# Performance work log

Measured on AMD Instinct MI355X. Metric: run time of the kernel, lower is better.

Reference implementation:

```python
import jax, jax.numpy as jnp
import numpy as np

N_USERS = 100000
N_ITEMS = 50000
D = 64
N_LAYERS = 3
E_RAW = 2_000_000
B = 4096


def setup_inputs() -> dict:
    rng = np.random.RandomState(0)
    u = rng.randint(0, N_USERS, E_RAW).astype(np.int64)
    i = rng.randint(0, N_ITEMS, E_RAW).astype(np.int64)
    lin = np.unique(u * N_ITEMS + i)  # dedupe interactions like the dok_matrix would
    u = (lin // N_ITEMS).astype(np.int32)
    i = (lin % N_ITEMS).astype(np.int32)
    deg_u = np.bincount(u, minlength=N_USERS).astype(np.float64)
    deg_i = np.bincount(i, minlength=N_ITEMS).astype(np.float64)
    inv_u = np.where(deg_u > 0, 1.0 / np.sqrt(np.maximum(deg_u, 1.0)), 0.0)
    inv_i = np.where(deg_i > 0, 1.0 / np.sqrt(np.maximum(deg_i, 1.0)), 0.0)
    val = (inv_u[u] * inv_i[i]).astype(np.float32)  # D^-1/2 A D^-1/2 entries
    # symmetric bipartite Laplacian: user block rows then item block rows
    rows = np.concatenate([u, i + N_USERS]).astype(np.int32)
    cols = np.concatenate([i + N_USERS, u]).astype(np.int32)
    vals = np.concatenate([val, val])

    key = jax.random.key(0)
    k1, k2, k3, k4 = jax.random.split(key, 4)
    embeds = jax.random.normal(k1, (N_USERS + N_ITEMS, D), jnp.float32) * 0.1
    users = jax.random.randint(k2, (B,), 0, N_USERS)
    pos_items = jax.random.randint(k3, (B,), 0, N_ITEMS)
    neg_items = jax.random.randint(k4, (B,), 0, N_ITEMS)
    return dict(embeds=embeds, vals=jnp.asarray(vals), rows=jnp.asarray(rows),
                cols=jnp.asarray(cols), users=users, pos_items=pos_items,
                neg_items=neg_items)


def reference(embeds, vals, rows, cols, users, pos_items, neg_items):
    N = N_USERS + N_ITEMS
    cur = embeds
    acc = embeds  # running sum over layer embeddings (incl. layer 0)
    for _ in range(N_LAYERS):
        msg = vals[:, None] * cur[cols]                      # [nnz, D] gather
        cur = jax.ops.segment_sum(msg, rows, num_segments=N)  # SpMM scatter-add
        acc = acc + cur
    mean = acc / (N_LAYERS + 1)
    user_e = mean[:N_USERS]
    item_e = mean[N_USERS:]
    return user_e[users], item_e[pos_items], item_e[neg_items]
```

## Files before the change

### kernel.cpp

```cpp
#include <hip/hip_runtime.h>
#include <hip/hip_bf16.h>

#define N_USERS 100000
#define N_ITEMS 50000
#define N_TOT   150000
#define D       64
#define NBUCK   ((N_ITEMS + 127) >> 7)
#define BCAP    6144
#define CONVU_B 391
#define FLAG_B  48

typedef float v2f __attribute__((ext_vector_type(2)));

__device__ __forceinline__ unsigned bf16rn(float f) {
    unsigned x = __float_as_uint(f);
    return (x + 0x7FFFu + ((x >> 16) & 1u)) >> 16;
}
__device__ __forceinline__ unsigned packbf(float a, float b) {
    return bf16rn(a) | (bf16rn(b) << 16);
}
__device__ __forceinline__ int lower_bound(const int* __restrict__ a, int n, int key) {
    int lo = 0, hi = n;
    while (lo < hi) {
        int mid = (lo + hi) >> 1;
        if (a[mid] < key) lo = mid + 1; else hi = mid;
    }
    return lo;
}

__global__ __launch_bounds__(256) void preA_kernel(
        const float* __restrict__ embeds, const int* __restrict__ rows,
        const int* __restrict__ cols, int* __restrict__ user_ptr,
        unsigned* __restrict__ ebfS, float* __restrict__ invrow,
        const int* __restrict__ users, const int* __restrict__ pos,
        const int* __restrict__ neg, unsigned char* __restrict__ flags,
        int* __restrict__ ccur, int* __restrict__ tmp,
        unsigned short* __restrict__ cols16, int E, int B) {
    int b = blockIdx.x, t = threadIdx.x;
    if (b < CONVU_B) {
        __shared__ int ptr_s[257];
        __shared__ float inv_s[256];
        int base = b * 256;
        int r = base + t;
        int v = lower_bound(rows, E, r);
        ptr_s[t] = v;
        if (r <= N_USERS) user_ptr[r] = v;
        if (t == 0) ptr_s[256] = lower_bound(rows, E, base + 256);
        __syncthreads();
        if (r < N_USERS) {
            int deg = ptr_s[t + 1] - ptr_s[t];
            float inv = (deg > 0) ? (float)(1.0 / sqrt((double)deg)) : 0.f;
            inv_s[t] = inv;
            invrow[r] = inv;
        } else inv_s[t] = 0.f;
        __syncthreads();
        int fl = t & 15;
        #pragma unroll
        for (int i = 0; i < 16; ++i) {
            int lr = i * 16 + (t >> 4);
            int row = base + lr;
            if (row < N_USERS) {
                float inv = inv_s[lr];
                float4 v4 = *(const float4*)(embeds + (size_t)row * D + fl * 4);
                uint2 o;
                o.x = packbf(inv * v4.x, inv * v4.y);
                o.y = packbf(inv * v4.z, inv * v4.w);
                *(uint2*)(ebfS + (size_t)row * 32 + fl * 2) = o;
            }
        }
    } else if (b < CONVU_B + FLAG_B) {
        int k = (b - CONVU_B) * 256 + t;
        if (k < 3 * B) {
            int row;
            if (k < B)          row = users[k];
            else if (k < 2 * B) row = N_USERS + pos[k - B];
            else                row = N_USERS + neg[k - 2 * B];
            flags[row] = 1;
        }
    } else {
        __shared__ int cnt[NBUCK];
        __shared__ int basep[NBUCK];
        const int K = 16;
        int chunk = (b - CONVU_B - FLAG_B) * (256 * K);
        for (int i = t; i < NBUCK; i += 256) cnt[i] = 0;
        __syncthreads();
        int pk[K]; int bk[K];
        #pragma unroll
        for (int k = 0; k < K; ++k) {
            int e = chunk + k * 256 + t;
            if (e < E) {
                int i = cols[e] - N_USERS;
                cols16[e] = (unsigned short)i;
                bk[k] = i >> 7;
                pk[k] = ((i & 127) << 17) | rows[e];
                atomicAdd(&cnt[bk[k]], 1);
            } else bk[k] = -1;
        }
        __syncthreads();
        for (int i = t; i < NBUCK; i += 256) {
            int c = cnt[i];
            basep[i] = c ? atomicAdd(&ccur[i], c) : 0;
            cnt[i] = 0;
        }
        __syncthreads();
        #pragma unroll
        for (int k = 0; k < K; ++k) {
            if (bk[k] >= 0) {
                int pos2 = basep[bk[k]] + atomicAdd(&cnt[bk[k]], 1);
                if (pos2 < BCAP)
                    tmp[(size_t)bk[k] * BCAP + pos2] = pk[k];
            }
        }
    }
}

__global__ __launch_bounds__(256) void preB_kernel(
        const int* __restrict__ tmp, const int* __restrict__ ccur,
        const float* __restrict__ embeds,
        int* __restrict__ item_beg, int* __restrict__ item_end,
        int* __restrict__ nbr, unsigned* __restrict__ ebfS,
        unsigned* __restrict__ bb1, float* __restrict__ invrow) {
    int b = blockIdx.x, t = threadIdx.x;
    if (b == NBUCK) {
        if (t < 16) {
            *(uint2*)(ebfS + (size_t)N_TOT * 32 + t * 2) = make_uint2(0u, 0u);
            *(uint2*)(bb1  + (size_t)N_TOT * 32 + t * 2) = make_uint2(0u, 0u);
        }
        if (t == 0) invrow[N_TOT] = 0.f;
        return;
    }
    __shared__ int stage[BCAP];
    __shared__ int hist[128];
    __shared__ int scn[128];
    __shared__ int curs[128];
    __shared__ float inv_s[128];
    int n = ccur[b]; if (n > BCAP) n = BCAP;
    const int* src = tmp + (size_t)b * BCAP;
    if (t < 128) hist[t] = 0;
    __syncthreads();
    for (int p = t; p < n; p += 256) {
        int q = src[p];
        stage[p] = q;
        atomicAdd(&hist[q >> 17], 1);
    }
    __syncthreads();
    if (t < 128) scn[t] = hist[t];
    __syncthreads();
    for (int off = 1; off < 128; off <<= 1) {
        int x = (t < 128 && t >= off) ? scn[t - off] : 0;
        __syncthreads();
        if (t < 128) scn[t] += x;
        __syncthreads();
    }
    if (t < 128) {
        int excl = scn[t] - hist[t];
        curs[t] = excl;
        int gi = (b << 7) + t;
        float inv = (hist[t] > 0) ? (float)(1.0 / sqrt((double)hist[t])) : 0.f;
        inv_s[t] = inv;
        if (gi < N_ITEMS) {
            item_beg[gi] = b * BCAP + excl;
            item_end[gi] = b * BCAP + excl + hist[t];
            invrow[N_USERS + gi] = inv;
        }
    }
    __syncthreads();
    int* dst = nbr + (size_t)b * BCAP;
    for (int p = t; p < n; p += 256) {
        int q = stage[p];
        int pos = atomicAdd(&curs[q >> 17], 1);
        dst[pos] = q & 0x1FFFF;
    }
    int fl = t & 15;
    #pragma unroll
    for (int i = 0; i < 8; ++i) {
        int lr = i * 16 + (t >> 4);
        int gi = (b << 7) + lr;
        if (gi < N_ITEMS) {
            int row = N_USERS + gi;
            float inv = inv_s[lr];
            float4 v4 = *(const float4*)(embeds + (size_t)row * D + fl * 4);
            uint2 o;
            o.x = packbf(inv * v4.x, inv * v4.y);
            o.y = packbf(inv * v4.z, inv * v4.w);
            *(uint2*)(ebfS + (size_t)row * 32 + fl * 2) = o;
        }
    }
}

__global__ __launch_bounds__(256) void agg_kernel(
        const unsigned* __restrict__ gsrc,
        float* __restrict__ nxt, unsigned* __restrict__ nxtb,
        const float* __restrict__ invrow,
        const unsigned char* __restrict__ flags,
        const int* __restrict__ user_ptr, const unsigned short* __restrict__ cols16,
        const int* __restrict__ item_beg, const int* __restrict__ item_end,
        const int* __restrict__ nbr) {
    int wave = (int)((blockIdx.x * blockDim.x + threadIdx.x) >> 6);
    int lane = (int)(threadIdx.x & 63);
    if (wave >= N_TOT) return;
    int g  = lane >> 3;
    int fl = lane & 7;

    bool is_user = wave < N_USERS;
    int s, epos, dummy;
    const unsigned* sb;
    if (is_user) {
        s = user_ptr[wave]; epos = user_ptr[wave + 1];
        sb = gsrc + (size_t)N_USERS * 32; dummy = N_ITEMS;
    } else {
        int i = wave - N_USERS; s = item_beg[i]; epos = item_end[i];
        sb = gsrc; dummy = N_TOT;
    }

    v2f a0 = {0.f, 0.f}, a1 = {0.f, 0.f}, a2 = {0.f, 0.f}, a3 = {0.f, 0.f};

    for (int base = s; base < epos; base += 64) {
        int cnt = epos - base; if (cnt > 64) cnt = 64;
        int col = dummy;
        if (lane < cnt)
            col = is_user ? (int)cols16[base + lane] : nbr[base + lane];
        int tcount = (cnt + 7) >> 3;
        #pragma unroll 4
        for (int t = 0; t < tcount; ++t) {
            int c = __shfl(col, 8 * t + g);
            uint4 q = *(const uint4*)(sb + (size_t)c * 32 + fl * 4);
            v2f p0 = {__uint_as_float(q.x << 16), __uint_as_float(q.x & 0xFFFF0000u)};
            v2f p1 = {__uint_as_float(q.y << 16), __uint_as_float(q.y & 0xFFFF0000u)};
            v2f p2 = {__uint_as_float(q.z << 16), __uint_as_float(q.z & 0xFFFF0000u)};
            v2f p3 = {__uint_as_float(q.w << 16), __uint_as_float(q.w & 0xFFFF0000u)};
            a0 += p0; a1 += p1; a2 += p2; a3 += p3;
        }
    }
    float acc[8] = {a0.x, a0.y, a1.x, a1.y, a2.x, a2.y, a3.x, a3.y};
    #pragma unroll
    for (int j = 0; j < 8; ++j) {
        acc[j] += __shfl_xor(acc[j], 8);
        acc[j] += __shfl_xor(acc[j], 16);
        acc[j] += __shfl_xor(acc[j], 32);
    }
    if (lane < 8) {
        float inv = invrow[wave];
        float f[8];
        #pragma unroll
        for (int j = 0; j < 8; ++j) f[j] = inv * acc[j];
        uint4 o;
        o.x = packbf(inv * f[0], inv * f[1]); o.y = packbf(inv * f[2], inv * f[3]);
        o.z = packbf(inv * f[4], inv * f[5]); o.w = packbf(inv * f[6], inv * f[7]);
        *(uint4*)(nxtb + (size_t)wave * 32 + fl * 4) = o;
        if (flags[wave]) {
            size_t ro = (size_t)wave * D + fl * 8;
            *(float4*)(nxt + ro)     = make_float4(f[0], f[1], f[2], f[3]);
            *(float4*)(nxt + ro + 4) = make_float4(f[4], f[5], f[6], f[7]);
        }
    }
}

__global__ __launch_bounds__(256) void agg3_fused_kernel(
        const unsigned* __restrict__ gsrc,
        const float* __restrict__ e0, const float* __restrict__ e1,
        const float* __restrict__ e2, const float* __restrict__ invrow,
        const int* __restrict__ users, const int* __restrict__ pos,
        const int* __restrict__ neg,
        const int* __restrict__ user_ptr, const unsigned short* __restrict__ cols16,
        const int* __restrict__ item_beg, const int* __restrict__ item_end,
        const int* __restrict__ nbr,
        float* __restrict__ out, int B) {
    int slot = (int)((blockIdx.x * blockDim.x + threadIdx.x) >> 6);
    int lane = (int)(threadIdx.x & 63);
    if (slot >= 3 * B) return;
    int g  = lane >> 3;
    int fl = lane & 7;

    int row;
    if (slot < B)          row = users[slot];
    else if (slot < 2 * B) row = N_USERS + pos[slot - B];
    else                   row = N_USERS + neg[slot - 2 * B];

    bool is_user = row < N_USERS;
    int s, epos, dummy;
    const unsigned* sb;
    if (is_user) {
        s = user_ptr[row]; epos = user_ptr[row + 1];
        sb = gsrc + (size_t)N_USERS * 32; dummy = N_ITEMS;
    } else {
        int i = row - N_USERS; s = item_beg[i]; epos = item_end[i];
        sb = gsrc; dummy = N_TOT;
    }

    v2f a0 = {0.f, 0.f}, a1 = {0.f, 0.f}, a2 = {0.f, 0.f}, a3 = {0.f, 0.f};

    for (int base = s; base < epos; base += 64) {
        int cnt = epos - base; if (cnt > 64) cnt = 64;
        int col = dummy;
        if (lane < cnt)
            col = is_user ? (int)cols16[base + lane] : nbr[base + lane];
        int tcount = (cnt + 7) >> 3;
        #pragma unroll 4
        for (int t = 0; t < tcount; ++t) {
            int c = __shfl(col, 8 * t + g);
            uint4 q = *(const uint4*)(sb + (size_t)c * 32 + fl * 4);
            v2f p0 = {__uint_as_float(q.x << 16), __uint_as_float(q.x & 0xFFFF0000u)};
            v2f p1 = {__uint_as_float(q.y << 16), __uint_as_float(q.y & 0xFFFF0000u)};
            v2f p2 = {__uint_as_float(q.z << 16), __uint_as_float(q.z & 0xFFFF0000u)};
            v2f p3 = {__uint_as_float(q.w << 16), __uint_as_float(q.w & 0xFFFF0000u)};
            a0 += p0; a1 += p1; a2 += p2; a3 += p3;
        }
    }
    float acc[8] = {a0.x, a0.y, a1.x, a1.y, a2.x, a2.y, a3.x, a3.y};
    #pragma unroll
    for (int j = 0; j < 8; ++j) {
        acc[j] += __shfl_xor(acc[j], 8);
        acc[j] += __shfl_xor(acc[j], 16);
        acc[j] += __shfl_xor(acc[j], 32);
    }
    if (lane < 8) {
        float inv = invrow[row];
        size_t ro = (size_t)row * D + fl * 8;
        float4 x0 = *(const float4*)(e0 + ro), x1 = *(const float4*)(e0 + ro + 4);
        float4 y0 = *(const float4*)(e1 + ro), y1 = *(const float4*)(e1 + ro + 4);
        float4 z0 = *(const float4*)(e2 + ro), z1 = *(const float4*)(e2 + ro + 4);
        float4 r0, r1;
        r0.x = (x0.x + y0.x + z0.x + inv * acc[0]) * 0.25f;
        r0.y = (x0.y + y0.y + z0.y + inv * acc[1]) * 0.25f;
        r0.z = (x0.z + y0.z + z0.z + inv * acc[2]) * 0.25f;
        r0.w = (x0.w + y0.w + z0.w + inv * acc[3]) * 0.25f;
        r1.x = (x1.x + y1.x + z1.x + inv * acc[4]) * 0.25f;
        r1.y = (x1.y + y1.y + z1.y + inv * acc[5]) * 0.25f;
        r1.z = (x1.z + y1.z + z1.z + inv * acc[6]) * 0.25f;
        r1.w = (x1.w + y1.w + z1.w + inv * acc[7]) * 0.25f;
        size_t oo = (size_t)slot * D + fl * 8;
        *(float4*)(out + oo)     = r0;
        *(float4*)(out + oo + 4) = r1;
    }
}

extern "C" void kernel_launch(void* const* d_in, const int* in_sizes, int n_in,
                              void* d_out, int out_size, void* d_ws, size_t ws_size,
                              hipStream_t stream) {
    const float* embeds = (const float*)d_in[0];
    const int*   rows   = (const int*)d_in[2];
    const int*   cols   = (const int*)d_in[3];
    const int*   users  = (const int*)d_in[4];
    const int*   pos    = (const int*)d_in[5];
    const int*   neg    = (const int*)d_in[6];
    const int E2 = in_sizes[1];
    const int E  = E2 / 2;
    const int B  = in_sizes[4];

    char* ws = (char*)d_ws;
    size_t off = 0;
    auto alloc = [&](size_t bytes) { void* p = ws + off; off = (off + bytes + 255) & ~(size_t)255; return p; };
    float*    buf1     = (float*)   alloc((size_t)N_TOT * D * sizeof(float));
    float*    buf2     = (float*)   alloc((size_t)N_TOT * D * sizeof(float));
    unsigned* ebfS     = (unsigned*)alloc((size_t)(N_TOT + 1) * 32 * sizeof(unsigned));
    unsigned* bb1      = (unsigned*)alloc((size_t)(N_TOT + 1) * 32 * sizeof(unsigned));
    int*      nbr      = (int*)     alloc((size_t)NBUCK * BCAP * sizeof(int));
    unsigned short* cols16 = (unsigned short*)alloc((size_t)E * sizeof(unsigned short));
    int*      user_ptr = (int*)     alloc((size_t)(N_USERS + 1) * sizeof(int));
    int*      ccur     = (int*)     alloc((size_t)NBUCK * sizeof(int));
    int*      item_beg = (int*)     alloc((size_t)N_ITEMS * sizeof(int));
    int*      item_end = (int*)     alloc((size_t)N_ITEMS * sizeof(int));
    float*    invrow   = (float*)   alloc((size_t)(N_TOT + 1) * sizeof(float));
    unsigned char* flags = (unsigned char*)alloc((size_t)N_TOT);
    int*      tmp      = (int*)buf1;

    hipMemsetAsync(ccur, 0, (size_t)NBUCK * sizeof(int), stream);
    hipMemsetAsync(flags, 0, (size_t)N_TOT, stream);
    const int scatB = (E + 4095) / 4096;
    preA_kernel<<<CONVU_B + FLAG_B + scatB, 256, 0, stream>>>(
        embeds, rows, cols, user_ptr, ebfS, invrow, users, pos, neg, flags,
        ccur, tmp, cols16, E, B);
    preB_kernel<<<NBUCK + 1, 256, 0, stream>>>(
        tmp, ccur, embeds, item_beg, item_end, nbr, ebfS, bb1, invrow);

    const int blocks = (N_TOT + 3) / 4;
    agg_kernel<<<blocks, 256, 0, stream>>>(ebfS, buf1, bb1, invrow, flags, user_ptr,
                                           cols16, item_beg, item_end, nbr);
    agg_kernel<<<blocks, 256, 0, stream>>>(bb1, buf2, ebfS, invrow, flags, user_ptr,
                                           cols16, item_beg, item_end, nbr);

    agg3_fused_kernel<<<(3 * B + 3) / 4, 256, 0, stream>>>(
        ebfS, embeds, buf1, buf2, invrow, users, pos, neg,
        user_ptr, cols16, item_beg, item_end, nbr, (float*)d_out, B);
}
```

Measured before the change: 338.8 us.

## Widen item buckets to 256 and stage scatter entries in shared memory

```diff
diff --git a/kernel.cpp b/kernel.cpp
--- a/kernel.cpp
+++ b/kernel.cpp
@@ -5,10 +5,11 @@
 #define N_ITEMS 50000
 #define N_TOT   150000
 #define D       64
-#define NBUCK   ((N_ITEMS + 127) >> 7)
-#define BCAP    6144
+#define NBUCK   ((N_ITEMS + 255) >> 8)
+#define BCAP    12288
 #define CONVU_B 391
 #define FLAG_B  48
+#define SCAT_K  32
 
 typedef float v2f __attribute__((ext_vector_type(2)));
 
@@ -78,37 +79,41 @@
             flags[row] = 1;
         }
     } else {
+        __shared__ int ebuf[256 * SCAT_K];
+        __shared__ unsigned char bbuf[256 * SCAT_K];
         __shared__ int cnt[NBUCK];
         __shared__ int basep[NBUCK];
-        const int K = 16;
-        int chunk = (b - CONVU_B - FLAG_B) * (256 * K);
-        for (int i = t; i < NBUCK; i += 256) cnt[i] = 0;
-        __syncthreads();
-        int pk[K]; int bk[K];
-        #pragma unroll
-        for (int k = 0; k < K; ++k) {
+        int chunk = (b - CONVU_B - FLAG_B) * (256 * SCAT_K);
+        if (t < NBUCK) cnt[t] = 0;
+        __syncthreads();
+        #pragma unroll 4
+        for (int k = 0; k < SCAT_K; ++k) {
             int e = chunk + k * 256 + t;
+            int idx = k * 256 + t;
             if (e < E) {
                 int i = cols[e] - N_USERS;
                 cols16[e] = (unsigned short)i;
-                bk[k] = i >> 7;
-                pk[k] = ((i & 127) << 17) | rows[e];
-                atomicAdd(&cnt[bk[k]], 1);
-            } else bk[k] = -1;
-        }
-        __syncthreads();
-        for (int i = t; i < NBUCK; i += 256) {
-            int c = cnt[i];
-            basep[i] = c ? atomicAdd(&ccur[i], c) : 0;
-            cnt[i] = 0;
-        }
-        __syncthreads();
-        #pragma unroll
-        for (int k = 0; k < K; ++k) {
-            if (bk[k] >= 0) {
-                int pos2 = basep[bk[k]] + atomicAdd(&cnt[bk[k]], 1);
+                int bu = i >> 8;
+                ebuf[idx] = ((i & 255) << 17) | rows[e];
+                bbuf[idx] = (unsigned char)bu;
+                atomicAdd(&cnt[bu], 1);
+            } else bbuf[idx] = 255;
+        }
+        __syncthreads();
+        if (t < NBUCK) {
+            int c = cnt[t];
+            basep[t] = c ? atomicAdd(&ccur[t], c) : 0;
+            cnt[t] = 0;
+        }
+        __syncthreads();
+        #pragma unroll 4
+        for (int k = 0; k < SCAT_K; ++k) {
+            int idx = k * 256 + t;
+            int bu = bbuf[idx];
+            if (bu < NBUCK) {
+                int pos2 = basep[bu] + atomicAdd(&cnt[bu], 1);
                 if (pos2 < BCAP)
-                    tmp[(size_t)bk[k] * BCAP + pos2] = pk[k];
+                    tmp[(size_t)bu * BCAP + pos2] = ebuf[idx];
             }
         }
     }
@@ -130,13 +135,13 @@
         return;
     }
     __shared__ int stage[BCAP];
-    __shared__ int hist[128];
-    __shared__ int scn[128];
-    __shared__ int curs[128];
-    __shared__ float inv_s[128];
+    __shared__ int hist[256];
+    __shared__ int scn[256];
+    __shared__ int curs[256];
+    __shared__ float inv_s[256];
     int n = ccur[b]; if (n > BCAP) n = BCAP;
     const int* src = tmp + (size_t)b * BCAP;
-    if (t < 128) hist[t] = 0;
+    hist[t] = 0;
     __syncthreads();
     for (int p = t; p < n; p += 256) {
         int q = src[p];
@@ -144,18 +149,18 @@
         atomicAdd(&hist[q >> 17], 1);
     }
     __syncthreads();
-    if (t < 128) scn[t] = hist[t];
+    scn[t] = hist[t];
     __syncthreads();
-    for (int off = 1; off < 128; off <<= 1) {
-        int x = (t < 128 && t >= off) ? scn[t - off] : 0;
-        __syncthreads();
-        if (t < 128) scn[t] += x;
-        __syncthreads();
-    }
-    if (t < 128) {
+    for (int off = 1; off < 256; off <<= 1) {
+        int x = (t >= off) ? scn[t - off] : 0;
+        __syncthreads();
+        scn[t] += x;
+        __syncthreads();
+    }
+    {
         int excl = scn[t] - hist[t];
         curs[t] = excl;
-        int gi = (b << 7) + t;
+        int gi = (b << 8) + t;
         float inv = (hist[t] > 0) ? (float)(1.0 / sqrt((double)hist[t])) : 0.f;
         inv_s[t] = inv;
         if (gi < N_ITEMS) {
@@ -173,9 +178,9 @@
     }
     int fl = t & 15;
     #pragma unroll
-    for (int i = 0; i < 8; ++i) {
+    for (int i = 0; i < 16; ++i) {
         int lr = i * 16 + (t >> 4);
-        int gi = (b << 7) + lr;
+        int gi = (b << 8) + lr;
         if (gi < N_ITEMS) {
             int row = N_USERS + gi;
             float inv = inv_s[lr];
@@ -367,7 +372,7 @@
 
     hipMemsetAsync(ccur, 0, (size_t)NBUCK * sizeof(int), stream);
     hipMemsetAsync(flags, 0, (size_t)N_TOT, stream);
-    const int scatB = (E + 4095) / 4096;
+    const int scatB = (E + 256 * SCAT_K - 1) / (256 * SCAT_K);
     preA_kernel<<<CONVU_B + FLAG_B + scatB, 256, 0, stream>>>(
         embeds, rows, cols, user_ptr, ebfS, invrow, users, pos, neg, flags,
         ccur, tmp, cols16, E, B);
```

After: 331.3 us. 2.2% less time.
